# Performance work log

Hardware: AMD Instinct MI355X
Metric: run time of the kernel (lower is better)

The kernel has to match this reference:

```python
import jax, jax.numpy as jnp
import numpy as np

N_EMBD = 1024
N_HEAD = 16
BLOCK_SIZE = 2048
NEG_INF = -1e10


def _rope_cache(head_dim, max_positions):
    # theta_i = 10000^{-2i/dim}, freqs[t, i] = t * theta_i
    theta = 1.0 / (10000.0 ** (jnp.arange(0, head_dim, 2, dtype=jnp.float32) / head_dim))
    freqs = jnp.arange(max_positions, dtype=jnp.float32)[:, None] * theta[None, :]
    return jnp.cos(freqs), jnp.sin(freqs)  # each (max_positions, head_dim//2)


def _apply_rope(x, cos, sin):
    # x: (B, nh, T, hs) interpreted as interleaved complex pairs
    B, nh, T, hs = x.shape
    xr = x.reshape(B, nh, T, hs // 2, 2)
    x0, x1 = xr[..., 0], xr[..., 1]
    c = cos[:T][None, None, :, :]
    s = sin[:T][None, None, :, :]
    o0 = x0 * c - x1 * s
    o1 = x0 * s + x1 * c
    return jnp.stack([o0, o1], axis=-1).reshape(B, nh, T, hs)


def setup_inputs() -> dict:
    key = jax.random.key(0)
    ks = jax.random.split(key, 9)
    B, T, C = 2, 2048, N_EMBD
    sc = 1.0 / np.sqrt(C)
    return {
        "x": jax.random.normal(ks[0], (B, T, C), jnp.float32),
        "Wq": jax.random.normal(ks[1], (C, C), jnp.float32) * sc,
        "bq": jax.random.normal(ks[2], (C,), jnp.float32) * 0.02,
        "Wk": jax.random.normal(ks[3], (C, C), jnp.float32) * sc,
        "bk": jax.random.normal(ks[4], (C,), jnp.float32) * 0.02,
        "Wv": jax.random.normal(ks[5], (C, C), jnp.float32) * sc,
        "bv": jax.random.normal(ks[6], (C,), jnp.float32) * 0.02,
        "Wp": jax.random.normal(ks[7], (C, C), jnp.float32) * sc,
        "bp": jax.random.normal(ks[8], (C,), jnp.float32) * 0.02,
    }


def reference(x, Wq, bq, Wk, bk, Wv, bv, Wp, bp):
    B, T, C = x.shape
    nh, hs = N_HEAD, C // N_HEAD

    def heads(W, b):
        return (x @ W.T + b).reshape(B, T, nh, hs).transpose(0, 2, 1, 3)

    q = heads(Wq, bq)
    k = heads(Wk, bk)
    v = heads(Wv, bv)

    cos, sin = _rope_cache(hs, BLOCK_SIZE)
    q = _apply_rope(q, cos, sin)
    k = _apply_rope(k, cos, sin)

    att = jnp.einsum("bhqd,bhkd->bhqk", q, k) * (1.0 / np.sqrt(hs))
    causal = jnp.tril(jnp.ones((T, T), dtype=bool))
    att = jnp.where(causal[None, None], att, NEG_INF)
    att = jax.nn.softmax(att, axis=-1)
    y = jnp.einsum("bhqk,bhkd->bhqd", att, v)
    y = y.transpose(0, 2, 1, 3).reshape(B, T, C)
    return y @ Wp.T + bp
```

## Files before the change

### kernel.cpp

```cpp
#include <hip/hip_runtime.h>

typedef __bf16 bf16;
typedef short  s16;
typedef s16   s16x8 __attribute__((ext_vector_type(8)));
typedef bf16  bf16x4 __attribute__((ext_vector_type(4)));
typedef float f32x4 __attribute__((ext_vector_type(4)));

#define B_SZ 2
#define T_SEQ 2048
#define C_DIM 1024
#define NH 16
#define HS 64
#define M_TOT (B_SZ * T_SEQ)

#define NEG_BIG (-30000.0f)
#define LOG2_10000 13.287712379549449f
#define Q_PRESCALE 0.18033688011112042f

__device__ __forceinline__ float san(float x) {
    unsigned u = __float_as_uint(x);
    return ((u & 0x7F800000u) == 0x7F800000u) ? 0.f : x;
}

__device__ __forceinline__ void load16_lds(const bf16* g, void* lds_base) {
    __builtin_amdgcn_global_load_lds(
        (const __attribute__((address_space(1))) void*)g,
        (__attribute__((address_space(3))) void*)lds_base, 16, 0, 0);
}

__global__ __launch_bounds__(256) void cvt_bf16_kernel(
    const float* __restrict__ x,  const float* __restrict__ wq,
    const float* __restrict__ wk, const float* __restrict__ wv,
    const float* __restrict__ wp,
    bf16* __restrict__ xb, bf16* __restrict__ wqb, bf16* __restrict__ wkb,
    bf16* __restrict__ wvb, bf16* __restrict__ wpb,
    float* __restrict__ cs, float* __restrict__ sn)
{
    const int z = blockIdx.y;
    if (z == 5) {
        const int idx = blockIdx.x * 256 + threadIdx.x;
        if (idx >= 65536) return;
        const int t = idx >> 5, i = idx & 31;
        const float theta = __builtin_exp2f(-(float)(2 * i) * (LOG2_10000 / 64.f));
        const float a = (float)t * theta;
        cs[idx] = san(cosf(a));
        sn[idx] = san(sinf(a));
        return;
    }
    const float* src = (z == 0) ? x : (z == 1) ? wq : (z == 2) ? wk : (z == 3) ? wv : wp;
    bf16* dst = (z == 0) ? xb : (z == 1) ? wqb : (z == 2) ? wkb : (z == 3) ? wvb : wpb;
    const int n = (z == 0) ? (M_TOT * C_DIM) : (C_DIM * C_DIM);

    const int i = (blockIdx.x * 256 + threadIdx.x) * 4;
    if (i >= n) return;
    const float4 v = *(const float4*)(src + i);
    bf16x4 o;
    o[0] = (bf16)v.x; o[1] = (bf16)v.y; o[2] = (bf16)v.z; o[3] = (bf16)v.w;
    *(bf16x4*)(dst + i) = o;
}

#define GEMM_CORE(Xp, Wp_)                                                     \
    const int t = threadIdx.x;                                                 \
    const int w = t >> 6;                                                      \
    const int lane = t & 63;                                                   \
    const int qd = lane >> 4;                                                  \
    const int r  = lane & 15;                                                  \
    const int wm = w & 1, wn = w >> 1;                                         \
    const int srow = t >> 2;                                                   \
    const int scol = (t & 3) * 8;                                              \
    const bf16* gA0 = (Xp) + (size_t)(m0 + srow) * C_DIM + scol;               \
    const bf16* gA1 = (Xp) + (size_t)(m0 + 64 + srow) * C_DIM + scol;          \
    const bf16* gB0 = (Wp_) + (size_t)(n0 + srow) * C_DIM + scol;              \
    const bf16* gB1 = (Wp_) + (size_t)(n0 + 64 + srow) * C_DIM + scol;         \
    char* ldsA0 = (char*)sA + (size_t)(w * 64) * 16;                           \
    char* ldsA1 = (char*)sA + (size_t)(256 + w * 64) * 16;                     \
    char* ldsB0 = (char*)sB + (size_t)(w * 64) * 16;                           \
    char* ldsB1 = (char*)sB + (size_t)(256 + w * 64) * 16;                     \
    f32x4 acc[4][4] = {};                                                      \
    for (int k0 = 0; k0 < C_DIM; k0 += 32) {                                   \
        __syncthreads();                                                       \
        load16_lds(gA0 + k0, ldsA0);                                           \
        load16_lds(gA1 + k0, ldsA1);                                           \
        load16_lds(gB0 + k0, ldsB0);                                           \
        load16_lds(gB1 + k0, ldsB1);                                           \
        __syncthreads();                                                       \
        s16x8 af[4], bfr[4];                                                   \
        _Pragma("unroll")                                                      \
        for (int mt = 0; mt < 4; mt++)                                         \
            af[mt] = *(const s16x8*)(sA + (wm * 64 + mt * 16 + r) * 32 + qd * 8); \
        _Pragma("unroll")                                                      \
        for (int nt = 0; nt < 4; nt++)                                         \
            bfr[nt] = *(const s16x8*)(sB + (wn * 64 + nt * 16 + r) * 32 + qd * 8); \
        _Pragma("unroll")                                                      \
        for (int mt = 0; mt < 4; mt++)                                         \
            _Pragma("unroll")                                                  \
            for (int nt = 0; nt < 4; nt++)                                     \
                acc[mt][nt] = __builtin_amdgcn_mfma_f32_16x16x32_bf16(         \
                    af[mt], bfr[nt], acc[mt][nt], 0, 0, 0);                    \
    }

__global__ __launch_bounds__(256) void qkv_gemm(
    const bf16* __restrict__ X,
    const bf16* __restrict__ Wq, const float* __restrict__ bq,
    const bf16* __restrict__ Wk, const float* __restrict__ bk,
    const bf16* __restrict__ Wv, const float* __restrict__ bv,
    const float* __restrict__ cs_tab, const float* __restrict__ sn_tab,
    bf16* __restrict__ q_ws, bf16* __restrict__ k_ws, bf16* __restrict__ vt_ws)
{
    __shared__ __attribute__((aligned(16))) bf16 sA[128 * 32];
    __shared__ __attribute__((aligned(16))) bf16 sB[128 * 32];

    const int mode = blockIdx.z;
    const bf16*  Wm   = (mode == 0) ? Wq : (mode == 1) ? Wk : Wv;
    const float* bias = (mode == 0) ? bq : (mode == 1) ? bk : bv;
    const int m0 = blockIdx.x * 128;
    const int n0 = blockIdx.y * 128;

    GEMM_CORE(X, Wm)

    if (mode == 2) {
        #pragma unroll
        for (int mt = 0; mt < 4; mt++) {
            const int mrow0 = m0 + wm * 64 + mt * 16 + qd * 4;
            const int bb = mrow0 >> 11;
            const int t0 = mrow0 & 2047;
            #pragma unroll
            for (int nt = 0; nt < 4; nt++) {
                const int col = n0 + wn * 64 + nt * 16 + r;
                const int h = col >> 6, d = col & 63;
                const float bv_ = bias[col];
                bf16x4 pk;
                #pragma unroll
                for (int reg = 0; reg < 4; reg++)
                    pk[reg] = (bf16)san(acc[mt][nt][reg] + bv_);
                *(bf16x4*)(vt_ws + ((size_t)(bb * NH + h) * HS + d) * T_SEQ + t0) = pk;
            }
        }
    } else {
        bf16* out = (mode == 0) ? q_ws : k_ws;
        const float post = (mode == 0) ? Q_PRESCALE : 1.0f;
        #pragma unroll
        for (int mt = 0; mt < 4; mt++) {
            const int mrow0 = m0 + wm * 64 + mt * 16 + qd * 4;
            const int bb = mrow0 >> 11;
            const int t0 = mrow0 & 2047;
            #pragma unroll
            for (int nt = 0; nt < 4; nt++) {
                const int col = n0 + wn * 64 + nt * 16 + r;
                const int h = col >> 6, d = col & 63;
                const int pi = d >> 1;
                const float bv_ = bias[col];
                #pragma unroll
                for (int reg = 0; reg < 4; reg++) {
                    const int tt = t0 + reg;
                    float v = san(acc[mt][nt][reg] + bv_);
                    float partner = __shfl_xor(v, 1);
                    float c = cs_tab[tt * 32 + pi];
                    float s = sn_tab[tt * 32 + pi];
                    float rot = (d & 1) ? (v * c + partner * s)
                                        : (v * c - partner * s);
                    out[((size_t)(bb * NH + h) * T_SEQ + tt) * HS + d] =
                        (bf16)san(rot * post);
                }
            }
        }
    }
}

__global__ __launch_bounds__(256) void proj_gemm(
    const bf16* __restrict__ Y, const bf16* __restrict__ Wp,
    const float* __restrict__ bp, float* __restrict__ out)
{
    __shared__ __attribute__((aligned(16))) bf16 sA[128 * 32];
    __shared__ __attribute__((aligned(16))) bf16 sB[128 * 32];

    const int m0 = blockIdx.x * 128;
    const int n0 = blockIdx.y * 128;

    GEMM_CORE(Y, Wp)

    #pragma unroll
    for (int mt = 0; mt < 4; mt++) {
        const int mrow0 = m0 + wm * 64 + mt * 16 + qd * 4;
        #pragma unroll
        for (int nt = 0; nt < 4; nt++) {
            const int col = n0 + wn * 64 + nt * 16 + r;
            const float bv_ = bp[col];
            #pragma unroll
            for (int reg = 0; reg < 4; reg++)
                out[(size_t)(mrow0 + reg) * C_DIM + col] = san(acc[mt][nt][reg] + bv_);
        }
    }
}

__global__ __launch_bounds__(256) void attn_kernel(
    const bf16* __restrict__ q_ws, const bf16* __restrict__ k_ws,
    const bf16* __restrict__ vt_ws, bf16* __restrict__ y_ws)
{
    __shared__ __attribute__((aligned(16))) bf16 sK[2][2][64][32];
    __shared__ __attribute__((aligned(16))) bf16 sV[2][2][64][32];
    __shared__ __attribute__((aligned(16))) bf16 sP[4][16][72];

    const int id = (int)(blockIdx.x + gridDim.x * blockIdx.y);
    const int bh = (id & 7) + 8 * (id >> 7);
    const int bx = (id >> 3) & 15;

    const int w    = threadIdx.x >> 6;
    const int lane = threadIdx.x & 63;
    const int qd = lane >> 4;
    const int r  = lane & 15;

    const bf16* Qb = q_ws + (size_t)bh * T_SEQ * HS;
    const bf16* Kb = k_ws + (size_t)bh * T_SEQ * HS;
    const bf16* Vb = vt_ws + (size_t)bh * HS * T_SEQ;

    const int srow = lane >> 2;
    const int scol = (lane & 3) * 8;
    const bf16* Kb_w = Kb + (size_t)(w * 16 + srow) * HS + scol;
    const bf16* Vb_w = Vb + (size_t)(w * 16 + srow) * T_SEQ + scol;

    bf16 (*pw)[72] = sP[w];
    const int bb = bh >> 4, h = bh & 15;

    #pragma unroll 1
    for (int phase = 0; phase < 2; phase++) {
        const int qt = phase ? bx : (T_SEQ / 64 - 1 - bx);
        const int q0 = qt * 64 + w * 16;

        s16x8 aq0 = *(const s16x8*)(Qb + (size_t)(q0 + r) * HS + qd * 8);
        s16x8 aq1 = *(const s16x8*)(Qb + (size_t)(q0 + r) * HS + 32 + qd * 8);

        f32x4 o[4] = {};
        float l_lane = 0.f;

        __syncthreads();
        load16_lds(Kb_w,      &sK[0][0][w * 16][0]);
        load16_lds(Kb_w + 32, &sK[0][1][w * 16][0]);
        load16_lds(Vb_w,      &sV[0][0][w * 16][0]);
        load16_lds(Vb_w + 32, &sV[0][1][w * 16][0]);

        for (int kt = 0; kt <= qt; kt++) {
            const int cur = kt & 1;
            __syncthreads();

            if (kt < qt) {
                const bf16* kp = Kb_w + (size_t)(kt + 1) * 64 * HS;
                const bf16* vp = Vb_w + (kt + 1) * 64;
                load16_lds(kp,      &sK[cur ^ 1][0][w * 16][0]);
                load16_lds(kp + 32, &sK[cur ^ 1][1][w * 16][0]);
                load16_lds(vp,      &sV[cur ^ 1][0][w * 16][0]);
                load16_lds(vp + 32, &sV[cur ^ 1][1][w * 16][0]);
            }

            f32x4 s[4];
            #pragma unroll
            for (int c = 0; c < 4; c++) {
                s16x8 k0 = *(const s16x8*)&sK[cur][0][c * 16 + r][qd * 8];
                s16x8 k1 = *(const s16x8*)&sK[cur][1][c * 16 + r][qd * 8];
                f32x4 z = {};
                z = __builtin_amdgcn_mfma_f32_16x16x32_bf16(k0, aq0, z, 0, 0, 0);
                z = __builtin_amdgcn_mfma_f32_16x16x32_bf16(k1, aq1, z, 0, 0, 0);
                s[c] = z;
            }

            if (kt == qt) {
                const int qg = q0 + r;
                #pragma unroll
                for (int c = 0; c < 4; c++)
                    #pragma unroll
                    for (int reg = 0; reg < 4; reg++) {
                        const int kg = kt * 64 + c * 16 + qd * 4 + reg;
                        s[c][reg] = (kg <= qg) ? s[c][reg] : NEG_BIG;
                    }
            }

            #pragma unroll
            for (int c = 0; c < 4; c++) {
                bf16x4 pk;
                #pragma unroll
                for (int reg = 0; reg < 4; reg++) {
                    float p = __builtin_exp2f(s[c][reg]);
                    l_lane += p;
                    pk[reg] = (bf16)p;
                }
                *(bf16x4*)&pw[r][c * 16 + qd * 4] = pk;
            }

            s16x8 ap0 = *(const s16x8*)&pw[r][qd * 8];
            s16x8 ap1 = *(const s16x8*)&pw[r][32 + qd * 8];
            #pragma unroll
            for (int nt = 0; nt < 4; nt++) {
                s16x8 av0 = *(const s16x8*)&sV[cur][0][nt * 16 + r][qd * 8];
                s16x8 av1 = *(const s16x8*)&sV[cur][1][nt * 16 + r][qd * 8];
                o[nt] = __builtin_amdgcn_mfma_f32_16x16x32_bf16(av0, ap0, o[nt], 0, 0, 0);
                o[nt] = __builtin_amdgcn_mfma_f32_16x16x32_bf16(av1, ap1, o[nt], 0, 0, 0);
            }
        }

        float l = l_lane;
        l += __shfl_xor(l, 16);
        l += __shfl_xor(l, 32);
        const float inv = 1.f / fmaxf(l, 1e-20f);

        const int q = q0 + r;
        bf16* dst = y_ws + ((size_t)(bb * T_SEQ + q) * NH + h) * HS;
        #pragma unroll
        for (int nt = 0; nt < 4; nt++) {
            bf16x4 pk;
            #pragma unroll
            for (int reg = 0; reg < 4; reg++)
                pk[reg] = (bf16)san(o[nt][reg] * inv);
            *(bf16x4*)(dst + nt * 16 + qd * 4) = pk;
        }
    }
}

extern "C" void kernel_launch(void* const* d_in, const int* in_sizes, int n_in,
                              void* d_out, int out_size, void* d_ws, size_t ws_size,
                              hipStream_t stream)
{
    const size_t MB = 1024 * 1024;
    const size_t NEED = 40 * MB + 2 * 65536 * sizeof(float);
    if (ws_size < NEED || n_in < 9) return;

    const float* x  = (const float*)d_in[0];
    const float* Wq = (const float*)d_in[1];
    const float* bq = (const float*)d_in[2];
    const float* Wk = (const float*)d_in[3];
    const float* bk = (const float*)d_in[4];
    const float* Wv = (const float*)d_in[5];
    const float* bv = (const float*)d_in[6];
    const float* Wp = (const float*)d_in[7];
    const float* bp = (const float*)d_in[8];
    float* out = (float*)d_out;

    char* ws = (char*)d_ws;
    bf16*  q_ws   = (bf16*)(ws + 0 * MB);
    bf16*  k_ws   = (bf16*)(ws + 8 * MB);
    bf16*  vt_ws  = (bf16*)(ws + 16 * MB);
    bf16*  x_b    = (bf16*)(ws + 24 * MB);
    bf16*  y_ws   = (bf16*)(ws + 24 * MB);
    bf16*  Wq_b   = (bf16*)(ws + 32 * MB);
    bf16*  Wk_b   = (bf16*)(ws + 34 * MB);
    bf16*  Wv_b   = (bf16*)(ws + 36 * MB);
    bf16*  Wp_b   = (bf16*)(ws + 38 * MB);
    float* cs_tab = (float*)(ws + 40 * MB);
    float* sn_tab = cs_tab + 65536;

    cvt_bf16_kernel<<<dim3(M_TOT * C_DIM / 4 / 256, 6), 256, 0, stream>>>(
        x, Wq, Wk, Wv, Wp, x_b, Wq_b, Wk_b, Wv_b, Wp_b, cs_tab, sn_tab);
    qkv_gemm<<<dim3(M_TOT / 128, C_DIM / 128, 3), 256, 0, stream>>>(
        x_b, Wq_b, bq, Wk_b, bk, Wv_b, bv, cs_tab, sn_tab, q_ws, k_ws, vt_ws);
    attn_kernel<<<dim3(T_SEQ / 128, B_SZ * NH), 256, 0, stream>>>(
        q_ws, k_ws, vt_ws, y_ws);
    proj_gemm<<<dim3(M_TOT / 128, C_DIM / 128), 256, 0, stream>>>(
        y_ws, Wp_b, bp, out);
}
```

Measured before the change: 207.9 us.

## Fuse Q/K/V projections into one kernel sharing X tiles, with double-buffered LDS

Replaces the three-way z-dimension QKV GEMM with a single kernel in which each block loads one 128-row X tile and multiplies it against 64-column slices of Wq, Wk and Wv. X is then read from memory once instead of three times. The kernel also double-buffers the LDS stages, so the next k-slice is loaded while the current one is computed, and it needs one barrier per iteration. In exchange, each thread holds 24 accumulators, which raises register pressure, and the grid has fewer, heavier blocks.

```diff
diff --git a/kernel.cpp b/kernel.cpp
--- a/kernel.cpp
+++ b/kernel.cpp
@@ -57,6 +57,123 @@
     bf16x4 o;
     o[0] = (bf16)v.x; o[1] = (bf16)v.y; o[2] = (bf16)v.z; o[3] = (bf16)v.w;
     *(bf16x4*)(dst + i) = o;
+}
+
+__global__ __launch_bounds__(256) void qkv_fused(
+    const bf16* __restrict__ X,
+    const bf16* __restrict__ Wq, const float* __restrict__ bq,
+    const bf16* __restrict__ Wk, const float* __restrict__ bk,
+    const bf16* __restrict__ Wv, const float* __restrict__ bv,
+    const float* __restrict__ cs_tab, const float* __restrict__ sn_tab,
+    bf16* __restrict__ q_ws, bf16* __restrict__ k_ws, bf16* __restrict__ vt_ws)
+{
+    __shared__ __attribute__((aligned(16))) bf16 sA[2][128 * 32];
+    __shared__ __attribute__((aligned(16))) bf16 sB[3][2][64 * 32];
+
+    const int m0 = blockIdx.x * 128;
+    const int n0 = blockIdx.y * 64;
+    const int t = threadIdx.x;
+    const int w = t >> 6;
+    const int lane = t & 63;
+    const int qd = lane >> 4;
+    const int r  = lane & 15;
+    const int wm = w & 1, wn = w >> 1;
+    const int srow = t >> 2;
+    const int scol = (t & 3) * 8;
+
+    const bf16* gA0 = X  + (size_t)(m0 + srow) * C_DIM + scol;
+    const bf16* gA1 = X  + (size_t)(m0 + 64 + srow) * C_DIM + scol;
+    const bf16* gBq = Wq + (size_t)(n0 + srow) * C_DIM + scol;
+    const bf16* gBk = Wk + (size_t)(n0 + srow) * C_DIM + scol;
+    const bf16* gBv = Wv + (size_t)(n0 + srow) * C_DIM + scol;
+
+    f32x4 acc[3][4][2] = {};
+
+    auto stage = [&](int k0, int buf) {
+        char* aBase = (char*)&sA[buf][0] + w * 1024;
+        load16_lds(gA0 + k0, aBase);
+        load16_lds(gA1 + k0, aBase + 4096);
+        load16_lds(gBq + k0, (char*)&sB[0][buf][0] + w * 1024);
+        load16_lds(gBk + k0, (char*)&sB[1][buf][0] + w * 1024);
+        load16_lds(gBv + k0, (char*)&sB[2][buf][0] + w * 1024);
+    };
+
+    stage(0, 0);
+
+    for (int k0 = 0; k0 < C_DIM; k0 += 32) {
+        const int cur = (k0 >> 5) & 1;
+        __syncthreads();
+
+        if (k0 + 32 < C_DIM) stage(k0 + 32, cur ^ 1);
+
+        s16x8 af[4], bfm[3][2];
+        #pragma unroll
+        for (int mt = 0; mt < 4; mt++)
+            af[mt] = *(const s16x8*)&sA[cur][(wm * 64 + mt * 16 + r) * 32 + qd * 8];
+        #pragma unroll
+        for (int m = 0; m < 3; m++)
+            #pragma unroll
+            for (int nt = 0; nt < 2; nt++)
+                bfm[m][nt] = *(const s16x8*)&sB[m][cur][(wn * 32 + nt * 16 + r) * 32 + qd * 8];
+
+        #pragma unroll
+        for (int m = 0; m < 3; m++)
+            #pragma unroll
+            for (int mt = 0; mt < 4; mt++)
+                #pragma unroll
+                for (int nt = 0; nt < 2; nt++)
+                    acc[m][mt][nt] = __builtin_amdgcn_mfma_f32_16x16x32_bf16(
+                        af[mt], bfm[m][nt], acc[m][mt][nt], 0, 0, 0);
+    }
+
+    #pragma unroll
+    for (int m = 0; m < 2; m++) {
+        const float* bias = m ? bk : bq;
+        bf16* out = m ? k_ws : q_ws;
+        const float post = m ? 1.0f : Q_PRESCALE;
+        #pragma unroll
+        for (int mt = 0; mt < 4; mt++) {
+            const int mrow0 = m0 + wm * 64 + mt * 16 + qd * 4;
+            const int bb = mrow0 >> 11;
+            const int t0 = mrow0 & 2047;
+            #pragma unroll
+            for (int nt = 0; nt < 2; nt++) {
+                const int col = n0 + wn * 32 + nt * 16 + r;
+                const int h = col >> 6, d = col & 63;
+                const int pi = d >> 1;
+                const float bv_ = bias[col];
+                #pragma unroll
+                for (int reg = 0; reg < 4; reg++) {
+                    const int tt = t0 + reg;
+                    float v = san(acc[m][mt][nt][reg] + bv_);
+                    float partner = __shfl_xor(v, 1);
+                    float c = cs_tab[tt * 32 + pi];
+                    float s = sn_tab[tt * 32 + pi];
+                    float rot = (d & 1) ? (v * c + partner * s)
+                                        : (v * c - partner * s);
+                    out[((size_t)(bb * NH + h) * T_SEQ + tt) * HS + d] =
+                        (bf16)san(rot * post);
+                }
+            }
+        }
+    }
+    #pragma unroll
+    for (int mt = 0; mt < 4; mt++) {
+        const int mrow0 = m0 + wm * 64 + mt * 16 + qd * 4;
+        const int bb = mrow0 >> 11;
+        const int t0 = mrow0 & 2047;
+        #pragma unroll
+        for (int nt = 0; nt < 2; nt++) {
+            const int col = n0 + wn * 32 + nt * 16 + r;
+            const int h = col >> 6, d = col & 63;
+            const float bv_ = bv[col];
+            bf16x4 pk;
+            #pragma unroll
+            for (int reg = 0; reg < 4; reg++)
+                pk[reg] = (bf16)san(acc[2][mt][nt][reg] + bv_);
+            *(bf16x4*)(vt_ws + ((size_t)(bb * NH + h) * HS + d) * T_SEQ + t0) = pk;
+        }
+    }
 }
 
 #define GEMM_CORE(Xp, Wp_)                                                     \
@@ -99,74 +216,6 @@
                     af[mt], bfr[nt], acc[mt][nt], 0, 0, 0);                    \
     }
 
-__global__ __launch_bounds__(256) void qkv_gemm(
-    const bf16* __restrict__ X,
-    const bf16* __restrict__ Wq, const float* __restrict__ bq,
-    const bf16* __restrict__ Wk, const float* __restrict__ bk,
-    const bf16* __restrict__ Wv, const float* __restrict__ bv,
-    const float* __restrict__ cs_tab, const float* __restrict__ sn_tab,
-    bf16* __restrict__ q_ws, bf16* __restrict__ k_ws, bf16* __restrict__ vt_ws)
-{
-    __shared__ __attribute__((aligned(16))) bf16 sA[128 * 32];
-    __shared__ __attribute__((aligned(16))) bf16 sB[128 * 32];
-
-    const int mode = blockIdx.z;
-    const bf16*  Wm   = (mode == 0) ? Wq : (mode == 1) ? Wk : Wv;
-    const float* bias = (mode == 0) ? bq : (mode == 1) ? bk : bv;
-    const int m0 = blockIdx.x * 128;
-    const int n0 = blockIdx.y * 128;
-
-    GEMM_CORE(X, Wm)
-
-    if (mode == 2) {
-        #pragma unroll
-        for (int mt = 0; mt < 4; mt++) {
-            const int mrow0 = m0 + wm * 64 + mt * 16 + qd * 4;
-            const int bb = mrow0 >> 11;
-            const int t0 = mrow0 & 2047;
-            #pragma unroll
-            for (int nt = 0; nt < 4; nt++) {
-                const int col = n0 + wn * 64 + nt * 16 + r;
-                const int h = col >> 6, d = col & 63;
-                const float bv_ = bias[col];
-                bf16x4 pk;
-                #pragma unroll
-                for (int reg = 0; reg < 4; reg++)
-                    pk[reg] = (bf16)san(acc[mt][nt][reg] + bv_);
-                *(bf16x4*)(vt_ws + ((size_t)(bb * NH + h) * HS + d) * T_SEQ + t0) = pk;
-            }
-        }
-    } else {
-        bf16* out = (mode == 0) ? q_ws : k_ws;
-        const float post = (mode == 0) ? Q_PRESCALE : 1.0f;
-        #pragma unroll
-        for (int mt = 0; mt < 4; mt++) {
-            const int mrow0 = m0 + wm * 64 + mt * 16 + qd * 4;
-            const int bb = mrow0 >> 11;
-            const int t0 = mrow0 & 2047;
-            #pragma unroll
-            for (int nt = 0; nt < 4; nt++) {
-                const int col = n0 + wn * 64 + nt * 16 + r;
-                const int h = col >> 6, d = col & 63;
-                const int pi = d >> 1;
-                const float bv_ = bias[col];
-                #pragma unroll
-                for (int reg = 0; reg < 4; reg++) {
-                    const int tt = t0 + reg;
-                    float v = san(acc[mt][nt][reg] + bv_);
-                    float partner = __shfl_xor(v, 1);
-                    float c = cs_tab[tt * 32 + pi];
-                    float s = sn_tab[tt * 32 + pi];
-                    float rot = (d & 1) ? (v * c + partner * s)
-                                        : (v * c - partner * s);
-                    out[((size_t)(bb * NH + h) * T_SEQ + tt) * HS + d] =
-                        (bf16)san(rot * post);
-                }
-            }
-        }
-    }
-}
-
 __global__ __launch_bounds__(256) void proj_gemm(
     const bf16* __restrict__ Y, const bf16* __restrict__ Wp,
     const float* __restrict__ bp, float* __restrict__ out)
@@ -349,7 +398,7 @@
 
     cvt_bf16_kernel<<<dim3(M_TOT * C_DIM / 4 / 256, 6), 256, 0, stream>>>(
         x, Wq, Wk, Wv, Wp, x_b, Wq_b, Wk_b, Wv_b, Wp_b, cs_tab, sn_tab);
-    qkv_gemm<<<dim3(M_TOT / 128, C_DIM / 128, 3), 256, 0, stream>>>(
+    qkv_fused<<<dim3(M_TOT / 128, C_DIM / 64), 256, 0, stream>>>(
         x_b, Wq_b, bq, Wk_b, bk, Wv_b, bv, cs_tab, sn_tab, q_ws, k_ws, vt_ws);
     attn_kernel<<<dim3(T_SEQ / 128, B_SZ * NH), 256, 0, stream>>>(
         q_ws, k_ws, vt_ws, y_ws);
```

Result: slower. 238.0 us (+14.4%).
